# Kernel tuning notes

Measured on AMD Instinct MI355X. Metric: run time of the kernel, lower is better.

## Reference

```python
import jax, jax.numpy as jnp
import numpy as np

T, N, B = 27, 16384, 256          # node types, nodes per type, batch size
IN_DIM, HID, OUT = 300, 128, 64


def setup_inputs() -> dict:
    key = jax.random.key(0)
    ks = jax.random.split(key, 6)
    feat = jax.random.normal(ks[0], (T, N, IN_DIM), dtype=jnp.float32)
    segment_ids = jnp.sort(
        jax.random.randint(ks[1], (T, N), 0, B, dtype=jnp.int64), axis=-1)
    W1 = jax.random.normal(ks[2], (T, IN_DIM, HID), dtype=jnp.float32) * 0.02
    b1 = jax.random.normal(ks[3], (T, HID), dtype=jnp.float32) * 0.02
    W2 = jax.random.normal(ks[4], (T, HID, OUT), dtype=jnp.float32) * 0.02
    b2 = jax.random.normal(ks[5], (T, OUT), dtype=jnp.float32) * 0.02
    return {"feat": feat, "segment_ids": segment_ids,
            "W1": W1, "b1": b1, "W2": W2, "b2": b2, "batch_size": B}


def _segment_mean(feat_t, seg_t, num_segments):
    # feat_t: [N, IN_DIM], seg_t: [N] sorted ids in [0, B)
    sums = jax.ops.segment_sum(feat_t, seg_t, num_segments=num_segments,
                               indices_are_sorted=True)          # [B, IN_DIM]
    cnts = jax.ops.segment_sum(jnp.ones((feat_t.shape[0],), feat_t.dtype),
                               seg_t, num_segments=num_segments,
                               indices_are_sorted=True)          # [B]
    # empty segments -> sum 0 / 1 = 0, matching the torch zeros fallback
    return sums / jnp.maximum(cnts, 1.0)[:, None]


def reference(feat, segment_ids, W1, b1, W2, b2, batch_size):
    # ragged per-(type, sample) mean pooling: [T, B, IN_DIM]
    pooled = jax.vmap(lambda f, s: _segment_mean(f, s, batch_size))(
        feat, segment_ids)
    # per-type 2-layer MLP (dropout is identity at inference)
    h = jax.nn.relu(jnp.einsum('tbi,tih->tbh', pooled, W1) + b1[:, None, :])
    out = jnp.einsum('tbh,tho->tbo', h, W2) + b2[:, None, :]
    # torch stacks per-type embeddings along dim=1 -> [B, T, OUT]
    return jnp.transpose(out, (1, 0, 2))
```

## Files before the change

kernel.cpp:

```cpp
#include <hip/hip_runtime.h>

#define T_TYPES 27
#define N_NODES 16384
#define B_BATCH 256
#define IN_DIM 300
#define HID 128
#define OUTD 64

#define RPB 32
#define VEC 75

__global__ __launch_bounds__(320) void pool_kernel(
    const float* __restrict__ feat,
    const int*   __restrict__ seg,
    float*       __restrict__ pooled)
{
    const int b = blockIdx.x;
    const int t = blockIdx.y;

    __shared__ int sBound[2];
    __shared__ float4 sAcc[4][80];

    if (threadIdx.x == 0 && threadIdx.y == 0) {
        const int* s = seg + (size_t)t * N_NODES;
        int lo = 0, hi = N_NODES;
        while (lo < hi) { int m = (lo + hi) >> 1; if (s[m] < b) lo = m + 1; else hi = m; }
        sBound[0] = lo;
        int lo2 = lo; hi = N_NODES;
        while (lo2 < hi) { int m = (lo2 + hi) >> 1; if (s[m] < b + 1) lo2 = m + 1; else hi = m; }
        sBound[1] = lo2;
    }
    __syncthreads();

    const int start = sBound[0];
    const int end   = sBound[1];
    const int x = threadIdx.x;
    const int y = threadIdx.y;

    float4 acc = make_float4(0.f, 0.f, 0.f, 0.f);
    if (x < VEC) {
        const float4* __restrict__ fv = (const float4*)feat;
        const size_t rowBase = (size_t)t * N_NODES;
        int n = start + y;
        for (; n + 12 < end; n += 16) {
            float4 v0 = fv[(rowBase + n     ) * VEC + x];
            float4 v1 = fv[(rowBase + n + 4 ) * VEC + x];
            float4 v2 = fv[(rowBase + n + 8 ) * VEC + x];
            float4 v3 = fv[(rowBase + n + 12) * VEC + x];
            acc.x += v0.x + v1.x + v2.x + v3.x;
            acc.y += v0.y + v1.y + v2.y + v3.y;
            acc.z += v0.z + v1.z + v2.z + v3.z;
            acc.w += v0.w + v1.w + v2.w + v3.w;
        }
        for (; n < end; n += 4) {
            float4 v = fv[(rowBase + n) * VEC + x];
            acc.x += v.x; acc.y += v.y; acc.z += v.z; acc.w += v.w;
        }
    }
    sAcc[y][x] = acc;
    __syncthreads();

    if (y == 0 && x < VEC) {
        float4 a0 = sAcc[0][x], a1 = sAcc[1][x], a2 = sAcc[2][x], a3 = sAcc[3][x];
        const int cnt = end - start;
        const float scale = (cnt > 0) ? (1.0f / (float)cnt) : 0.0f;
        float4 r;
        r.x = (a0.x + a1.x + a2.x + a3.x) * scale;
        r.y = (a0.y + a1.y + a2.y + a3.y) * scale;
        r.z = (a0.z + a1.z + a2.z + a3.z) * scale;
        r.w = (a0.w + a1.w + a2.w + a3.w) * scale;
        ((float4*)pooled)[((size_t)t * B_BATCH + b) * VEC + x] = r;
    }
}

__global__ __launch_bounds__(256) void mlp_kernel(
    const float* __restrict__ pooled,
    const float* __restrict__ W1,
    const float* __restrict__ b1,
    const float* __restrict__ W2,
    const float* __restrict__ b2,
    float*       __restrict__ out)
{
    const int t  = blockIdx.y;
    const int b0 = blockIdx.x * RPB;
    const int tid = threadIdx.x;

    __shared__ float sP[RPB][IN_DIM + 1];
    __shared__ float sH[RPB][HID + 1];

    {
        const float* __restrict__ psrc =
            pooled + ((size_t)t * B_BATCH + b0) * IN_DIM;
        for (int idx = tid; idx < RPB * IN_DIM; idx += 256) {
            int r = idx / IN_DIM;
            int i = idx - r * IN_DIM;
            sP[r][i] = psrc[idx];
        }
    }
    __syncthreads();

    {
        const int r  = tid & 31;
        const int hq = tid >> 5;
        float acc[16];
        {
            const float* __restrict__ bb = b1 + t * HID + hq * 16;
            #pragma unroll
            for (int j = 0; j < 16; ++j) acc[j] = bb[j];
        }
        const float* __restrict__ w1p =
            W1 + (size_t)t * IN_DIM * HID + hq * 16;
        #pragma unroll 2
        for (int i = 0; i < IN_DIM; ++i) {
            const float p = sP[r][i];
            const float4* __restrict__ w = (const float4*)(w1p + (size_t)i * HID);
            float4 wv[4];
            wv[0] = w[0]; wv[1] = w[1]; wv[2] = w[2]; wv[3] = w[3];
            #pragma unroll
            for (int q = 0; q < 4; ++q) {
                acc[q * 4 + 0] += p * wv[q].x;
                acc[q * 4 + 1] += p * wv[q].y;
                acc[q * 4 + 2] += p * wv[q].z;
                acc[q * 4 + 3] += p * wv[q].w;
            }
        }
        #pragma unroll
        for (int j = 0; j < 16; ++j)
            sH[r][hq * 16 + j] = fmaxf(acc[j], 0.0f);
    }
    __syncthreads();

    {
        const int r  = tid & 31;
        const int oq = tid >> 5;
        float acc[8];
        {
            const float* __restrict__ bb = b2 + t * OUTD + oq * 8;
            #pragma unroll
            for (int j = 0; j < 8; ++j) acc[j] = bb[j];
        }
        const float* __restrict__ w2p =
            W2 + (size_t)t * HID * OUTD + oq * 8;
        #pragma unroll 2
        for (int k = 0; k < HID; ++k) {
            const float h = sH[r][k];
            const float4* __restrict__ w = (const float4*)(w2p + (size_t)k * OUTD);
            float4 w0 = w[0], w1v = w[1];
            acc[0] += h * w0.x;  acc[1] += h * w0.y;
            acc[2] += h * w0.z;  acc[3] += h * w0.w;
            acc[4] += h * w1v.x; acc[5] += h * w1v.y;
            acc[6] += h * w1v.z; acc[7] += h * w1v.w;
        }
        float* __restrict__ op =
            out + ((size_t)(b0 + r) * T_TYPES + t) * OUTD + oq * 8;
        #pragma unroll
        for (int j = 0; j < 8; ++j) op[j] = acc[j];
    }
}

extern "C" void kernel_launch(void* const* d_in, const int* in_sizes, int n_in,
                              void* d_out, int out_size, void* d_ws, size_t ws_size,
                              hipStream_t stream) {
    const float* feat = (const float*)d_in[0];
    const int*   seg  = (const int*)  d_in[1];
    const float* W1   = (const float*)d_in[2];
    const float* b1   = (const float*)d_in[3];
    const float* W2   = (const float*)d_in[4];
    const float* b2   = (const float*)d_in[5];
    float* out = (float*)d_out;

    float* pooled = (float*)d_ws;

    dim3 g1(B_BATCH, T_TYPES), blk1(80, 4);
    hipLaunchKernelGGL(pool_kernel, g1, blk1, 0, stream, feat, seg, pooled);

    dim3 g2(B_BATCH / RPB, T_TYPES), blk2(256);
    hipLaunchKernelGGL(mlp_kernel, g2, blk2, 0, stream,
                       pooled, W1, b1, W2, b2, out);
}
```

Measured before the change: 775.6 us.

## Precompute segment bounds in a separate kernel and halve pool block rows

Adds a bounds_kernel that computes every segment start offset per type in parallel, replacing the serial single-thread binary searches at the start of each pool block. The pool kernel now reads its bounds from global memory, uses 2 row-groups instead of 4, and unrolls 8 loads per thread to keep memory-level parallelism. The cost is an extra kernel launch and a serial dependency between bounds and pooling, plus fewer threads per block in the bandwidth-bound reduction.

```diff
diff --git a/kernel.cpp b/kernel.cpp
--- a/kernel.cpp
+++ b/kernel.cpp
@@ -10,65 +10,71 @@
 #define RPB 32
 #define VEC 75
 
-__global__ __launch_bounds__(320) void pool_kernel(
+__global__ __launch_bounds__(256) void bounds_kernel(
+    const int* __restrict__ seg,
+    int*       __restrict__ bounds)
+{
+    const int t = blockIdx.x;
+    const int* __restrict__ s = seg + (size_t)t * N_NODES;
+    int* __restrict__ bt = bounds + t * (B_BATCH + 1);
+    for (int i = threadIdx.x; i <= N_NODES; i += 256) {
+        const int cur  = (i < N_NODES) ? s[i] : B_BATCH;
+        const int prev = (i > 0) ? s[i - 1] : -1;
+        for (int v = prev + 1; v <= cur; ++v) bt[v] = i;
+    }
+}
+
+__global__ __launch_bounds__(160) void pool_kernel(
     const float* __restrict__ feat,
-    const int*   __restrict__ seg,
+    const int*   __restrict__ bounds,
     float*       __restrict__ pooled)
 {
     const int b = blockIdx.x;
     const int t = blockIdx.y;
-
-    __shared__ int sBound[2];
-    __shared__ float4 sAcc[4][80];
-
-    if (threadIdx.x == 0 && threadIdx.y == 0) {
-        const int* s = seg + (size_t)t * N_NODES;
-        int lo = 0, hi = N_NODES;
-        while (lo < hi) { int m = (lo + hi) >> 1; if (s[m] < b) lo = m + 1; else hi = m; }
-        sBound[0] = lo;
-        int lo2 = lo; hi = N_NODES;
-        while (lo2 < hi) { int m = (lo2 + hi) >> 1; if (s[m] < b + 1) lo2 = m + 1; else hi = m; }
-        sBound[1] = lo2;
-    }
-    __syncthreads();
-
-    const int start = sBound[0];
-    const int end   = sBound[1];
     const int x = threadIdx.x;
     const int y = threadIdx.y;
+
+    const int start = bounds[t * (B_BATCH + 1) + b];
+    const int end   = bounds[t * (B_BATCH + 1) + b + 1];
+
+    __shared__ float4 sAcc[80];
 
     float4 acc = make_float4(0.f, 0.f, 0.f, 0.f);
     if (x < VEC) {
         const float4* __restrict__ fv = (const float4*)feat;
         const size_t rowBase = (size_t)t * N_NODES;
         int n = start + y;
-        for (; n + 12 < end; n += 16) {
+        for (; n + 14 < end; n += 16) {
             float4 v0 = fv[(rowBase + n     ) * VEC + x];
-            float4 v1 = fv[(rowBase + n + 4 ) * VEC + x];
-            float4 v2 = fv[(rowBase + n + 8 ) * VEC + x];
-            float4 v3 = fv[(rowBase + n + 12) * VEC + x];
-            acc.x += v0.x + v1.x + v2.x + v3.x;
-            acc.y += v0.y + v1.y + v2.y + v3.y;
-            acc.z += v0.z + v1.z + v2.z + v3.z;
-            acc.w += v0.w + v1.w + v2.w + v3.w;
+            float4 v1 = fv[(rowBase + n + 2 ) * VEC + x];
+            float4 v2 = fv[(rowBase + n + 4 ) * VEC + x];
+            float4 v3 = fv[(rowBase + n + 6 ) * VEC + x];
+            float4 v4 = fv[(rowBase + n + 8 ) * VEC + x];
+            float4 v5 = fv[(rowBase + n + 10) * VEC + x];
+            float4 v6 = fv[(rowBase + n + 12) * VEC + x];
+            float4 v7 = fv[(rowBase + n + 14) * VEC + x];
+            acc.x += ((v0.x + v1.x) + (v2.x + v3.x)) + ((v4.x + v5.x) + (v6.x + v7.x));
+            acc.y += ((v0.y + v1.y) + (v2.y + v3.y)) + ((v4.y + v5.y) + (v6.y + v7.y));
+            acc.z += ((v0.z + v1.z) + (v2.z + v3.z)) + ((v4.z + v5.z) + (v6.z + v7.z));
+            acc.w += ((v0.w + v1.w) + (v2.w + v3.w)) + ((v4.w + v5.w) + (v6.w + v7.w));
         }
-        for (; n < end; n += 4) {
+        for (; n < end; n += 2) {
             float4 v = fv[(rowBase + n) * VEC + x];
             acc.x += v.x; acc.y += v.y; acc.z += v.z; acc.w += v.w;
         }
     }
-    sAcc[y][x] = acc;
+    if (y == 1) sAcc[x] = acc;
     __syncthreads();
 
     if (y == 0 && x < VEC) {
-        float4 a0 = sAcc[0][x], a1 = sAcc[1][x], a2 = sAcc[2][x], a3 = sAcc[3][x];
+        const float4 a1 = sAcc[x];
         const int cnt = end - start;
         const float scale = (cnt > 0) ? (1.0f / (float)cnt) : 0.0f;
         float4 r;
-        r.x = (a0.x + a1.x + a2.x + a3.x) * scale;
-        r.y = (a0.y + a1.y + a2.y + a3.y) * scale;
-        r.z = (a0.z + a1.z + a2.z + a3.z) * scale;
-        r.w = (a0.w + a1.w + a2.w + a3.w) * scale;
+        r.x = (acc.x + a1.x) * scale;
+        r.y = (acc.y + a1.y) * scale;
+        r.z = (acc.z + a1.z) * scale;
+        r.w = (acc.w + a1.w) * scale;
         ((float4*)pooled)[((size_t)t * B_BATCH + b) * VEC + x] = r;
     }
 }
@@ -170,9 +176,13 @@
     float* out = (float*)d_out;
 
     float* pooled = (float*)d_ws;
+    int*   bounds = (int*)((char*)d_ws + (size_t)T_TYPES * B_BATCH * IN_DIM * 4);
 
-    dim3 g1(B_BATCH, T_TYPES), blk1(80, 4);
-    hipLaunchKernelGGL(pool_kernel, g1, blk1, 0, stream, feat, seg, pooled);
+    hipLaunchKernelGGL(bounds_kernel, dim3(T_TYPES), dim3(256), 0, stream,
+                       seg, bounds);
+
+    dim3 g1(B_BATCH, T_TYPES), blk1(80, 2);
+    hipLaunchKernelGGL(pool_kernel, g1, blk1, 0, stream, feat, bounds, pooled);
 
     dim3 g2(B_BATCH / RPB, T_TYPES), blk2(256);
     hipLaunchKernelGGL(mlp_kernel, g2, blk2, 0, stream,
```

Measured after the change: 812.9 us. +4.8%, slower.
